# Optimization experiments

Hardware: AMD Instinct MI355X
Metric: run time of the kernel (lower is better)

## Reference

```python
import jax, jax.numpy as jnp
import numpy as np

EMB = 512      # embedding / LSTM input size
HID = 1024     # LSTM hidden size per direction
NTAGS = 5      # output classes
NWORDS = 50257 # vocab size
T = 4096       # sequence length (batch is hard-coded to 1 in the original)


def setup_inputs() -> dict:
    key = jax.random.key(0)
    ks = jax.random.split(key, 13)
    f32 = jnp.float32

    def gauss(k, shape, scale=0.05):
        return jax.random.normal(k, shape, f32) * scale

    return {
        "words": jax.random.randint(ks[0], (T,), 0, NWORDS),
        # torch.nn.init.uniform_(word_emb.weight, -0.25, 0.25)
        "emb": jax.random.uniform(ks[1], (NWORDS, EMB), f32, -0.25, 0.25),
        # forward-direction LSTM params (PyTorch layout, gate order i,f,g,o)
        "Wih_f": gauss(ks[2], (4 * HID, EMB)),
        "Whh_f": gauss(ks[3], (4 * HID, HID)),
        "bih_f": gauss(ks[4], (4 * HID,)),
        "bhh_f": gauss(ks[5], (4 * HID,)),
        # backward-direction LSTM params
        "Wih_b": gauss(ks[6], (4 * HID, EMB)),
        "Whh_b": gauss(ks[7], (4 * HID, HID)),
        "bih_b": gauss(ks[8], (4 * HID,)),
        "bhh_b": gauss(ks[9], (4 * HID,)),
        # projection Linear(2*HID, NTAGS)
        "Wp": gauss(ks[10], (NTAGS, 2 * HID)),
        "bp": gauss(ks[11], (NTAGS,)),
    }


def _lstm_scan(x, Wih, Whh, bias):
    """Single-direction LSTM over x: [T, E] -> hidden states [T, H]."""
    H = Whh.shape[1]
    # precompute input-to-gate contributions for all timesteps: [T, 4H]
    xg = x @ Wih.T + bias

    def step(carry, g_in):
        h, c = carry
        gates = g_in + h @ Whh.T
        i, f, g, o = jnp.split(gates, 4)
        i = jax.nn.sigmoid(i)
        f = jax.nn.sigmoid(f)
        g = jnp.tanh(g)
        o = jax.nn.sigmoid(o)
        c = f * c + i * g
        h = o * jnp.tanh(c)
        return (h, c), h

    init = (jnp.zeros((H,), x.dtype), jnp.zeros((H,), x.dtype))
    _, hs = jax.lax.scan(step, init, xg)
    return hs


def reference(words, emb, Wih_f, Whh_f, bih_f, bhh_f,
              Wih_b, Whh_b, bih_b, bhh_b, Wp, bp):
    x = emb[words]                                        # [T, E]
    hf = _lstm_scan(x, Wih_f, Whh_f, bih_f + bhh_f)       # [T, H]
    hb = _lstm_scan(x[::-1], Wih_b, Whh_b, bih_b + bhh_b)[::-1]  # [T, H]
    # PyTorch bi-LSTM output[t] = concat(h_fwd[t], h_bwd[t]); take last step
    last = jnp.concatenate([hf[-1], hb[-1]])              # [2H]
    out = last @ Wp.T + bp                                # [NTAGS]
    return out[None, :]                                   # [1, NTAGS]
```

## Files before the change

### kernel.cpp

```cpp
#include <hip/hip_runtime.h>

typedef _Float16 half8 __attribute__((ext_vector_type(8)));
typedef float floatx4 __attribute__((ext_vector_type(4)));
typedef unsigned int u32;
typedef unsigned long long u64;
typedef u64 u64x2 __attribute__((ext_vector_type(2)));

#define T_SEQ 4096
#define EMBD  512
#define HID   1024
#define G4    4096
#define NWG   64


__device__ __forceinline__ void stage16(const void* g, void* l) {
  __builtin_amdgcn_global_load_lds((const __attribute__((address_space(1))) u32*)g,
                                   (__attribute__((address_space(3))) u32*)l, 16, 0, 0);
}

__device__ __forceinline__ float fsigmoid(float x) {
  return 1.f / (1.f + __expf(-x));
}
__device__ __forceinline__ float ftanh(float x) {
  x = fminf(fmaxf(x, -15.f), 15.f);
  float e = __expf(2.f * x);
  return (e - 1.f) / (e + 1.f);
}


__global__ __launch_bounds__(256) void prep_kernel(
    const float* __restrict__ Whh, const float* __restrict__ Wih,
    const float* __restrict__ emb, const int* __restrict__ words,
    const float* __restrict__ bih, const float* __restrict__ bhh,
    _Float16* __restrict__ whh_h, _Float16* __restrict__ wih_h,
    _Float16* __restrict__ xh, float* __restrict__ biasf, u64* __restrict__ hg) {
  const long long S1 = (long long)G4 * HID;
  const long long S2 = (long long)G4 * EMBD;
  const long long S3 = (long long)T_SEQ * EMBD;
  const long long S4 = G4;
  const long long S5 = 1024;
  const long long tot = S1 + S2 + S3 + S4 + S5;
  long long stride = (long long)gridDim.x * blockDim.x;
  for (long long i = (long long)blockIdx.x * blockDim.x + threadIdx.x; i < tot; i += stride) {
    long long j = i;
    if (j < S1) { whh_h[j] = (_Float16)Whh[j]; continue; }
    j -= S1;
    if (j < S2) { wih_h[j] = (_Float16)Wih[j]; continue; }
    j -= S2;
    if (j < S3) {
      int t = (int)(j >> 9), e = (int)(j & 511);
      xh[j] = (_Float16)emb[(long long)words[t] * EMBD + e];
      continue;
    }
    j -= S3;
    if (j < S4) { biasf[j] = bih[j] + bhh[j]; continue; }
    j -= S4;
    hg[j] = 0ull;
  }
}


__global__ __launch_bounds__(256) void xg_gemm(
    const _Float16* __restrict__ A, const _Float16* __restrict__ B,
    const float* __restrict__ biasf, float* __restrict__ C) {
  __shared__ char smem[2][2][8192];
  const int tid = threadIdx.x;
  const int lane = tid & 63;
  const int wid = tid >> 6;
  const int wy = wid >> 1, wx = wid & 1;
  const int tm = blockIdx.x * 128, tn = blockIdx.y * 128;

  floatx4 acc[4][4];
#pragma unroll
  for (int a = 0; a < 4; a++)
#pragma unroll
    for (int b = 0; b < 4; b++) acc[a][b] = (floatx4){0.f, 0.f, 0.f, 0.f};

  auto stage = [&](int buf, int kb) {
#pragma unroll
    for (int ii = 0; ii < 2; ii++) {
      int ci = tid + ii * 256;
      int r = ci >> 2, cs = ci & 3;
      int c = cs ^ (r & 3);
      const _Float16* srcA = A + (long long)(tm + r) * EMBD + kb + c * 8;
      const _Float16* srcB = B + (long long)(tn + r) * EMBD + kb + c * 8;
      char* ldsA = &smem[buf][0][(ci & ~63) << 4];
      char* ldsB = &smem[buf][1][(ci & ~63) << 4];
      stage16(srcA, ldsA);
      stage16(srcB, ldsB);
    }
  };

  stage(0, 0);
  __syncthreads();

  for (int t = 0; t < 16; t++) {
    int cur = t & 1;
    if (t < 15) stage(cur ^ 1, (t + 1) * 32);
    const char* As = smem[cur][0];
    const char* Bs = smem[cur][1];
    const int kc = lane >> 4;
    half8 af[4], bfr[4];
#pragma unroll
    for (int am = 0; am < 4; am++) {
      int r = wy * 64 + am * 16 + (lane & 15);
      af[am] = *(const half8*)(As + r * 64 + ((kc ^ (r & 3)) << 4));
    }
#pragma unroll
    for (int bn = 0; bn < 4; bn++) {
      int r = wx * 64 + bn * 16 + (lane & 15);
      bfr[bn] = *(const half8*)(Bs + r * 64 + ((kc ^ (r & 3)) << 4));
    }
#pragma unroll
    for (int am = 0; am < 4; am++)
#pragma unroll
      for (int bn = 0; bn < 4; bn++)
        acc[am][bn] = __builtin_amdgcn_mfma_f32_16x16x32_f16(af[am], bfr[bn], acc[am][bn], 0, 0, 0);
    __syncthreads();
  }

#pragma unroll
  for (int am = 0; am < 4; am++) {
    int mrow = tm + wy * 64 + am * 16 + (lane >> 4) * 4;
#pragma unroll
    for (int bn = 0; bn < 4; bn++) {
      int n = tn + wx * 64 + bn * 16 + (lane & 15);
      int r = n & 1023, g = n >> 10;
      int np = ((r >> 4) << 6) + (((r >> 2) & 3) << 4) + ((r & 3) << 2) + g;
      float bias = biasf[n];
#pragma unroll
      for (int rg = 0; rg < 4; rg++)
        C[(long long)(mrow + rg) * G4 + np] = acc[am][bn][rg] + bias;
    }
  }
}


__global__ __launch_bounds__(256, 1) void lstm_fwd(
    const _Float16* __restrict__ Whh_h, const float* __restrict__ xg,
    u64* __restrict__ hg) {
  __shared__ u32 hp[512];
  const int tid = threadIdx.x;
  const int lane = tid & 63;
  const int w = tid >> 6;
  const int wg = blockIdx.x;
  const int n = lane & 15;
  const int kc = lane >> 4;

  const int R = (n & 3) * HID + wg * 16 + w * 4 + (n >> 2);
  half8 Wb[32];
  {
    const _Float16* wr = Whh_h + (long long)R * HID + kc * 8;
#pragma unroll
    for (int kk = 0; kk < 32; kk++)
      Wb[kk] = *(const half8*)(wr + kk * 32);
  }

  u64* h0 = hg;
  u64* h1 = hg + 512;
  float c = 0.f;

  const float* xbase = xg + wg * 64 + w * 16 + lane;
  float xv_cur = 0.f, xv_nxt = 0.f;
  if (lane < 16) xv_cur = xbase[0];

  for (int s = 0; s < T_SEQ; s++) {
    const u64* src = (s & 1) ? h1 : h0;
    u64* dst = (s & 1) ? h0 : h1;

    {
      const u64* p = src + 2 * tid;
      const u32 want = (u32)s;
      u64 e0, e1;
      int spins = 0;
      for (;;) {
        u64x2 v;
        asm volatile("global_load_dwordx4 %0, %1, off sc1\n\ts_waitcnt vmcnt(0)"
                     : "=v"(v) : "v"(p) : "memory");
        if ((u32)(v.x >> 32) == want && (u32)(v.y >> 32) == want) { e0 = v.x; e1 = v.y; break; }
        if ((++spins & 15) == 0) {
          u64 a = __hip_atomic_load(p,     __ATOMIC_RELAXED, __HIP_MEMORY_SCOPE_AGENT);
          u64 b = __hip_atomic_load(p + 1, __ATOMIC_RELAXED, __HIP_MEMORY_SCOPE_AGENT);
          if ((u32)(a >> 32) == want && (u32)(b >> 32) == want) { e0 = a; e1 = b; break; }
        }
      }
      *reinterpret_cast<u64*>(&hp[2 * tid]) = ((u64)(u32)e1 << 32) | (u64)(u32)e0;
    }

    if (lane < 16 && s + 1 < T_SEQ) xv_nxt = xbase[(long long)(s + 1) * G4];

    __syncthreads();

    floatx4 ac0 = (floatx4){0.f,0.f,0.f,0.f};
    floatx4 ac1 = (floatx4){0.f,0.f,0.f,0.f};
    floatx4 ac2 = (floatx4){0.f,0.f,0.f,0.f};
    floatx4 ac3 = (floatx4){0.f,0.f,0.f,0.f};
    const char* hh = (const char*)hp;
#pragma unroll
    for (int kb = 0; kb < 8; kb++) {
      half8 a0 = *(const half8*)(hh + (kb * 4 + 0) * 64 + kc * 16);
      half8 a1 = *(const half8*)(hh + (kb * 4 + 1) * 64 + kc * 16);
      half8 a2 = *(const half8*)(hh + (kb * 4 + 2) * 64 + kc * 16);
      half8 a3 = *(const half8*)(hh + (kb * 4 + 3) * 64 + kc * 16);
      ac0 = __builtin_amdgcn_mfma_f32_16x16x32_f16(a0, Wb[kb * 4 + 0], ac0, 0, 0, 0);
      ac1 = __builtin_amdgcn_mfma_f32_16x16x32_f16(a1, Wb[kb * 4 + 1], ac1, 0, 0, 0);
      ac2 = __builtin_amdgcn_mfma_f32_16x16x32_f16(a2, Wb[kb * 4 + 2], ac2, 0, 0, 0);
      ac3 = __builtin_amdgcn_mfma_f32_16x16x32_f16(a3, Wb[kb * 4 + 3], ac3, 0, 0, 0);
    }
    float gv = ac0[0] + ac1[0] + ac2[0] + ac3[0] + xv_cur;

    float a = ((lane & 3) == 2) ? ftanh(gv) : fsigmoid(gv);
    int base = lane & ~3;
    float i_ = __shfl(a, base + 0);
    float f_ = __shfl(a, base + 1);
    float g_ = __shfl(a, base + 2);
    float o_ = __shfl(a, base + 3);
    c = f_ * c + i_ * g_;
    float hn = o_ * ftanh(c);

    union { _Float16 hx[2]; u32 u; } pk;
    pk.hx[0] = (_Float16)hn; pk.hx[1] = (_Float16)0.f;
    u32 bits = pk.u & 0xffffu;
    u32 nbr = (u32)__shfl((int)bits, lane | 4);
    if (lane < 16 && (lane & 7) == 0) {
      u64 pkt = ((u64)(u32)(s + 1) << 32) | (u64)(bits | ((nbr & 0xffffu) << 16));
      __hip_atomic_store(&dst[wg * 8 + w * 2 + (lane >> 3)], pkt,
                         __ATOMIC_RELAXED, __HIP_MEMORY_SCOPE_AGENT);
    }
    __syncthreads();
    xv_cur = xv_nxt;
  }
}


__global__ __launch_bounds__(256) void bwd_gates(
    const float* __restrict__ Wihb, const float* __restrict__ emb,
    const int* __restrict__ words, const float* __restrict__ bihb,
    const float* __restrict__ bhhb, float* __restrict__ gb) {
  const int row = blockIdx.x * 4 + (threadIdx.x >> 6);
  const int lane = threadIdx.x & 63;
  const long long wl = words[T_SEQ - 1];
  const float* xr = emb + wl * EMBD;
  const float* wr = Wihb + (long long)row * EMBD;
  const int k0 = lane * 8;
  float s = 0.f;
#pragma unroll
  for (int j = 0; j < 8; j += 4) {
    float4 wv = *(const float4*)(wr + k0 + j);
    float4 xv = *(const float4*)(xr + k0 + j);
    s += wv.x * xv.x + wv.y * xv.y + wv.z * xv.z + wv.w * xv.w;
  }
#pragma unroll
  for (int m = 1; m < 64; m <<= 1) s += __shfl_xor(s, m);
  if (lane == 0) gb[row] = s + bihb[row] + bhhb[row];
}


__global__ __launch_bounds__(256) void final_k(
    const u64* __restrict__ hg, const float* __restrict__ gb,
    const float* __restrict__ Wp, const float* __restrict__ bp,
    float* __restrict__ out) {
  __shared__ float last[2 * HID];
  __shared__ float red[4];
  const int tid = threadIdx.x;
  for (int p = tid; p < 512; p += 256) {
    u32 b = (u32)hg[p];
    union { unsigned short s; _Float16 h; } lo, hi;
    lo.s = (unsigned short)(b & 0xffffu);
    hi.s = (unsigned short)(b >> 16);
    last[2 * p]     = (float)lo.h;
    last[2 * p + 1] = (float)hi.h;
  }
  for (int j = tid; j < HID; j += 256) {
    float i_ = fsigmoid(gb[j]);
    float g_ = ftanh(gb[2 * HID + j]);
    float o_ = fsigmoid(gb[3 * HID + j]);
    float cb = i_ * g_;
    last[HID + j] = o_ * ftanh(cb);
  }
  __syncthreads();
  const int lane = tid & 63, wv = tid >> 6;
  for (int nn = 0; nn < 5; nn++) {
    float p = 0.f;
    for (int j = tid; j < 2 * HID; j += 256) p += last[j] * Wp[nn * 2 * HID + j];
#pragma unroll
    for (int m = 1; m < 64; m <<= 1) p += __shfl_xor(p, m);
    if (lane == 0) red[wv] = p;
    __syncthreads();
    if (tid == 0) out[nn] = red[0] + red[1] + red[2] + red[3] + bp[nn];
    __syncthreads();
  }
}


extern "C" void kernel_launch(void* const* d_in, const int* in_sizes, int n_in,
                              void* d_out, int out_size, void* d_ws, size_t ws_size,
                              hipStream_t stream) {
  const int*   words = (const int*)d_in[0];
  const float* emb   = (const float*)d_in[1];
  const float* Wih_f = (const float*)d_in[2];
  const float* Whh_f = (const float*)d_in[3];
  const float* bih_f = (const float*)d_in[4];
  const float* bhh_f = (const float*)d_in[5];
  const float* Wih_b = (const float*)d_in[6];
  const float* bih_b = (const float*)d_in[8];
  const float* bhh_b = (const float*)d_in[9];
  const float* Wp    = (const float*)d_in[10];
  const float* bp    = (const float*)d_in[11];
  float* out = (float*)d_out;

  char* ws = (char*)d_ws;
  float*    XG    = (float*)(ws);
  _Float16* WHH   = (_Float16*)(ws + 67108864);
  _Float16* WIH   = (_Float16*)(ws + 75497472);
  _Float16* XH    = (_Float16*)(ws + 79691776);
  u64*      HG    = (u64*)(ws + 83886080);
  float*    GB    = (float*)(ws + 83902464);
  float*    BIASF = (float*)(ws + 83918848);

  prep_kernel<<<2048, 256, 0, stream>>>(Whh_f, Wih_f, emb, words, bih_f, bhh_f,
                                        WHH, WIH, XH, BIASF, HG);
  xg_gemm<<<dim3(32, 32), 256, 0, stream>>>(XH, WIH, BIASF, XG);
  lstm_fwd<<<NWG, 256, 0, stream>>>(WHH, XG, HG);
  bwd_gates<<<1024, 256, 0, stream>>>(Wih_b, emb, words, bih_b, bhh_b, GB);
  final_k<<<1, 256, 0, stream>>>(HG, GB, Wp, bp, out);
}
```

Measured before the change: 6.711 ms.

## Double-buffer LDS hidden state, drop second barrier, pipeline spin-polling loads

Splits the shared hidden-state buffer in two so each step writes a different LDS buffer, which allows removing the trailing __syncthreads per timestep. The spin-wait on the global h packet now keeps two loads in flight with wave-wide __all checks, cutting polling latency. Gate activations become branch-free, using one exp and a fast reciprocal with per-lane multipliers, and the tanh clamp is dropped. The risks are subtle ordering hazards with a single barrier and slightly lower precision from the approximate rcp.

```diff
diff --git a/kernel.cpp b/kernel.cpp
--- a/kernel.cpp
+++ b/kernel.cpp
@@ -18,13 +18,19 @@
                                    (__attribute__((address_space(3))) u32*)l, 16, 0, 0);
 }
 
+__device__ __forceinline__ float frcp(float x) {
+#if __has_builtin(__builtin_amdgcn_rcpf)
+  return __builtin_amdgcn_rcpf(x);
+#else
+  return 1.f / x;
+#endif
+}
+
 __device__ __forceinline__ float fsigmoid(float x) {
-  return 1.f / (1.f + __expf(-x));
+  return frcp(1.f + __expf(-x));
 }
 __device__ __forceinline__ float ftanh(float x) {
-  x = fminf(fmaxf(x, -15.f), 15.f);
-  float e = __expf(2.f * x);
-  return (e - 1.f) / (e + 1.f);
+  return fmaf(2.f, frcp(1.f + __expf(-2.f * x)), -1.f);
 }
 
 
@@ -139,7 +145,7 @@
 __global__ __launch_bounds__(256, 1) void lstm_fwd(
     const _Float16* __restrict__ Whh_h, const float* __restrict__ xg,
     u64* __restrict__ hg) {
-  __shared__ u32 hp[512];
+  __shared__ u32 hp[2][512];
   const int tid = threadIdx.x;
   const int lane = tid & 63;
   const int w = tid >> 6;
@@ -159,43 +165,50 @@
   u64* h0 = hg;
   u64* h1 = hg + 512;
   float c = 0.f;
+  const float mulm = ((lane & 3) == 2) ? 2.f : 1.f;
+  const float addm = ((lane & 3) == 2) ? -1.f : 0.f;
 
   const float* xbase = xg + wg * 64 + w * 16 + lane;
-  float xv_cur = 0.f, xv_nxt = 0.f;
-  if (lane < 16) xv_cur = xbase[0];
+  float xv_cur = (lane < 16) ? xbase[0] : 0.f;
+  float xv_nxt = 0.f;
 
   for (int s = 0; s < T_SEQ; s++) {
-    const u64* src = (s & 1) ? h1 : h0;
+    const u64* p = ((s & 1) ? h1 : h0) + 2 * tid;
     u64* dst = (s & 1) ? h0 : h1;
-
-    {
-      const u64* p = src + 2 * tid;
-      const u32 want = (u32)s;
-      u64 e0, e1;
-      int spins = 0;
+    const u32 want = (u32)s;
+
+    u64x2 va, vb, got;
+    asm volatile("global_load_dwordx4 %0, %1, off sc1" : "=v"(va) : "v"(p) : "memory");
+    asm volatile("global_load_dwordx4 %0, %1, off sc1" : "=v"(vb) : "v"(p) : "memory");
+    asm volatile("s_waitcnt vmcnt(2)" ::: "memory");
+    __builtin_amdgcn_sched_barrier(0);
+    if (__all(((u32)(va.x >> 32) == want) & ((u32)(va.y >> 32) == want))) {
+      got = va;
+    } else {
+      asm volatile("global_load_dwordx4 %0, %1, off sc1" : "=v"(va) : "v"(p) : "memory");
       for (;;) {
-        u64x2 v;
-        asm volatile("global_load_dwordx4 %0, %1, off sc1\n\ts_waitcnt vmcnt(0)"
-                     : "=v"(v) : "v"(p) : "memory");
-        if ((u32)(v.x >> 32) == want && (u32)(v.y >> 32) == want) { e0 = v.x; e1 = v.y; break; }
-        if ((++spins & 15) == 0) {
-          u64 a = __hip_atomic_load(p,     __ATOMIC_RELAXED, __HIP_MEMORY_SCOPE_AGENT);
-          u64 b = __hip_atomic_load(p + 1, __ATOMIC_RELAXED, __HIP_MEMORY_SCOPE_AGENT);
-          if ((u32)(a >> 32) == want && (u32)(b >> 32) == want) { e0 = a; e1 = b; break; }
-        }
+        asm volatile("s_waitcnt vmcnt(1)" ::: "memory");
+        __builtin_amdgcn_sched_barrier(0);
+        if (__all(((u32)(vb.x >> 32) == want) & ((u32)(vb.y >> 32) == want))) { got = vb; break; }
+        asm volatile("global_load_dwordx4 %0, %1, off sc1" : "=v"(vb) : "v"(p) : "memory");
+        asm volatile("s_waitcnt vmcnt(1)" ::: "memory");
+        __builtin_amdgcn_sched_barrier(0);
+        if (__all(((u32)(va.x >> 32) == want) & ((u32)(va.y >> 32) == want))) { got = va; break; }
+        asm volatile("global_load_dwordx4 %0, %1, off sc1" : "=v"(va) : "v"(p) : "memory");
       }
-      *reinterpret_cast<u64*>(&hp[2 * tid]) = ((u64)(u32)e1 << 32) | (u64)(u32)e0;
-    }
-
-    if (lane < 16 && s + 1 < T_SEQ) xv_nxt = xbase[(long long)(s + 1) * G4];
-
-    __syncthreads();
+    }
+
+    u32* hb = hp[s & 1];
+    *reinterpret_cast<u64*>(&hb[2 * tid]) = ((u64)(u32)got.y << 32) | (u64)(u32)got.x;
+    asm volatile("s_waitcnt lgkmcnt(0)" ::: "memory");
+    __builtin_amdgcn_sched_barrier(0);
+    __builtin_amdgcn_s_barrier();
 
     floatx4 ac0 = (floatx4){0.f,0.f,0.f,0.f};
     floatx4 ac1 = (floatx4){0.f,0.f,0.f,0.f};
     floatx4 ac2 = (floatx4){0.f,0.f,0.f,0.f};
     floatx4 ac3 = (floatx4){0.f,0.f,0.f,0.f};
-    const char* hh = (const char*)hp;
+    const char* hh = (const char*)hb;
 #pragma unroll
     for (int kb = 0; kb < 8; kb++) {
       half8 a0 = *(const half8*)(hh + (kb * 4 + 0) * 64 + kc * 16);
@@ -207,16 +220,27 @@
       ac2 = __builtin_amdgcn_mfma_f32_16x16x32_f16(a2, Wb[kb * 4 + 2], ac2, 0, 0, 0);
       ac3 = __builtin_amdgcn_mfma_f32_16x16x32_f16(a3, Wb[kb * 4 + 3], ac3, 0, 0, 0);
     }
+
+    asm volatile("s_waitcnt vmcnt(0)" ::: "memory");
+    __builtin_amdgcn_sched_barrier(0);
+    asm volatile("" :: "v"(va), "v"(vb));
+
+    if (lane < 16) xv_nxt = xbase[(long long)((s + 1) & (T_SEQ - 1)) * G4];
+
     float gv = ac0[0] + ac1[0] + ac2[0] + ac3[0] + xv_cur;
 
-    float a = ((lane & 3) == 2) ? ftanh(gv) : fsigmoid(gv);
-    int base = lane & ~3;
-    float i_ = __shfl(a, base + 0);
-    float f_ = __shfl(a, base + 1);
-    float g_ = __shfl(a, base + 2);
-    float o_ = __shfl(a, base + 3);
-    c = f_ * c + i_ * g_;
-    float hn = o_ * ftanh(c);
+    float e = __expf(-(mulm * gv));
+    float t = frcp(1.f + e);
+    float a = fmaf(t, mulm, addm);
+    int base4 = lane & ~3;
+    float i_ = __shfl(a, base4 + 0);
+    float f_ = __shfl(a, base4 + 1);
+    float g_ = __shfl(a, base4 + 2);
+    float o_ = __shfl(a, base4 + 3);
+    c = fmaf(f_, c, i_ * g_);
+    float e2 = __expf(-2.f * c);
+    float th = fmaf(2.f, frcp(1.f + e2), -1.f);
+    float hn = o_ * th;
 
     union { _Float16 hx[2]; u32 u; } pk;
     pk.hx[0] = (_Float16)hn; pk.hx[1] = (_Float16)0.f;
@@ -227,7 +251,6 @@
       __hip_atomic_store(&dst[wg * 8 + w * 2 + (lane >> 3)], pkt,
                          __ATOMIC_RELAXED, __HIP_MEMORY_SCOPE_AGENT);
     }
-    __syncthreads();
     xv_cur = xv_nxt;
   }
 }
```

Measured after the change: 6.227 ms. -7.2%, faster.
